# Kernel optimization log

Measured on AMD Instinct MI355X. Metric: run time of the kernel, lower is better.

The kernel has to match this reference:

```python
import jax, jax.numpy as jnp
import numpy as np
import math

B, N, F_IN, F_OUT = 8, 2048, 128, 128


def _uniform(key, shape, stdv):
    return jax.random.uniform(key, shape, dtype=jnp.float32, minval=-stdv, maxval=stdv)


def setup_inputs() -> dict:
    key = jax.random.key(0)
    k_x, k_a, k_w, k_att, k_bw, k_ba = jax.random.split(key, 6)
    X = jax.random.normal(k_x, (B, N, F_IN), dtype=jnp.float32)
    # dense 0/1 adjacency, as consumed by torch.bmm(A, ...)
    A = jax.random.randint(k_a, (B, N, N), 0, 2).astype(jnp.float32)
    stdv_W = 1.0 / math.sqrt(F_OUT)        # W.size(1) == n_fea_out
    stdv_a = 1.0 / math.sqrt(2 * F_OUT)    # a.size(1) == 2*n_fea_out
    W = _uniform(k_w, (F_IN, F_OUT), stdv_W)
    a = _uniform(k_att, (1, 2 * F_OUT), stdv_a)
    bias_W = _uniform(k_bw, (F_OUT,), stdv_W)
    bias_a = _uniform(k_ba, (N,), stdv_a)
    return {"X": X, "A": A, "W": W, "a": a, "bias_a": bias_a, "bias_W": bias_W}


def reference(X, A, W, a, bias_a, bias_W):
    # XW: [B, N, F_out]
    XW = jnp.einsum('bnf,fo->bno', X, W)
    f = W.shape[1]
    # Original materializes Z[b,i,j] = concat(XW[b,j], XW[b,i]) then dots with a.
    # This is separable: Z1[b,i,j] = a[:f]@XW[b,j] + a[f:]@XW[b,i] + bias_a[j]
    a_j = a[0, :f]   # multiplies XW[b, j]
    a_i = a[0, f:]   # multiplies XW[b, i]
    s_j = jnp.einsum('bnf,f->bn', XW, a_j)  # [B, N]
    s_i = jnp.einsum('bnf,f->bn', XW, a_i)  # [B, N]
    Z1 = s_i[:, :, None] + s_j[:, None, :] + bias_a[None, None, :]  # [B, N, N]
    den = jnp.exp(Z1)
    num = jnp.einsum('bik,bkj->bij', A, den)  # torch.bmm(A, denominator)
    # where numerator == 0 the torch code leaves att uninitialized; use 0 deterministically
    nz = num != 0
    att = jnp.where(nz, den / jnp.where(nz, num, 1.0), 0.0)
    buf = jnp.einsum('bij,bjf->bif', att, XW)
    H = jnp.einsum('bij,bjf->bif', A, buf) + bias_W
    return H
```

## Files before the change

kernel.cpp:

```cpp
#include <hip/hip_runtime.h>

#define BB 8
#define NN 2048
#define FF 128


__global__ __launch_bounds__(256) void k1_p_xsum(const float* __restrict__ X,
                                                 const float* __restrict__ W,
                                                 const float* __restrict__ av,
                                                 float* __restrict__ p,
                                                 float* __restrict__ xpart) {
    __shared__ float wls[FF];
    __shared__ float xls[FF];
    const int t = threadIdx.x;
    if (t < FF) {
        const float4* W4 = (const float4*)(W + t * FF);
        const float4* a4 = (const float4*)(av + FF);
        float s = 0.f;
#pragma unroll
        for (int f = 0; f < FF / 4; ++f) {
            const float4 w4 = W4[f], aa = a4[f];
            s += w4.x * aa.x + w4.y * aa.y + w4.z * aa.z + w4.w * aa.w;
        }
        wls[t] = s;
        xls[t] = 0.f;
    }
    __syncthreads();

    const int gr0 = blockIdx.x * 32;
    const int lane = t & 63, wave = t >> 6;
    const int half = lane >> 5, l32 = lane & 31;
    const float4 wv = ((const float4*)wls)[l32];
    float4 cs = make_float4(0.f, 0.f, 0.f, 0.f);
    const float4* X4 = (const float4*)(X + (size_t)gr0 * FF);

#pragma unroll
    for (int it = 0; it < 4; ++it) {
        const int rloc = wave * 8 + it * 2 + half;
        const float4 xv = X4[(size_t)rloc * 32 + l32];
        cs.x += xv.x; cs.y += xv.y; cs.z += xv.z; cs.w += xv.w;
        float s = xv.x * wv.x + xv.y * wv.y + xv.z * wv.z + xv.w * wv.w;
#pragma unroll
        for (int off = 16; off; off >>= 1) s += __shfl_xor(s, off, 64);
        if (l32 == 0) p[gr0 + rloc] = expf(s);
    }

    atomicAdd(&xls[l32 * 4 + 0], cs.x);
    atomicAdd(&xls[l32 * 4 + 1], cs.y);
    atomicAdd(&xls[l32 * 4 + 2], cs.z);
    atomicAdd(&xls[l32 * 4 + 3], cs.w);
    __syncthreads();
    if (t < FF) xpart[blockIdx.x * FF + t] = xls[t];
}

__global__ __launch_bounds__(256) void k3_r(const float* __restrict__ A,
                                            const float* __restrict__ W,
                                            const float* __restrict__ xpart,
                                            const float* __restrict__ p,
                                            float* __restrict__ r,
                                            float* __restrict__ S,
                                            unsigned* __restrict__ pk) {
    __shared__ float p_lds[NN];
    const int t = threadIdx.x;

    if (blockIdx.x == 0) {
#pragma unroll
        for (int k = 0; k < 4; ++k) {
            const int o = t + 256 * k;
            const int b = o >> 7, f = o & 127;
            float s = 0.f;
            for (int j = 0; j < 64; ++j) s += xpart[(b * 64 + j) * FF + f];
            p_lds[o] = s;
        }
        __syncthreads();
#pragma unroll
        for (int k = 0; k < 4; ++k) {
            const int o = t + 256 * k;
            const int b = o >> 7, f = o & 127;
            float s = 0.f;
#pragma unroll 8
            for (int c = 0; c < FF; ++c) s += p_lds[b * FF + c] * W[c * FF + f];
            S[o] = s;
        }
        return;
    }

    const int row0 = (blockIdx.x - 1) * 8;
    const int b = row0 >> 11;
    const float4* p4 = (const float4*)(p + (size_t)b * NN);
    float4* pl4 = (float4*)p_lds;
    pl4[t]       = p4[t];
    pl4[t + 256] = p4[t + 256];
    __syncthreads();

    const int lane = t & 63, wave = t >> 6;
    const int rowA = row0 + wave * 2;
    const int rowB = rowA + 1;
    const float4* Aa = (const float4*)(A + (size_t)rowA * NN);
    const float4* Ab = (const float4*)(A + (size_t)rowB * NN);

    const float4 va0 = Aa[0 * 64 + lane], va1 = Aa[1 * 64 + lane];
    const float4 va2 = Aa[2 * 64 + lane], va3 = Aa[3 * 64 + lane];
    const float4 va4 = Aa[4 * 64 + lane], va5 = Aa[5 * 64 + lane];
    const float4 va6 = Aa[6 * 64 + lane], va7 = Aa[7 * 64 + lane];
    const float4 vb0 = Ab[0 * 64 + lane], vb1 = Ab[1 * 64 + lane];
    const float4 vb2 = Ab[2 * 64 + lane], vb3 = Ab[3 * 64 + lane];
    const float4 vb4 = Ab[4 * 64 + lane], vb5 = Ab[5 * 64 + lane];
    const float4 vb6 = Ab[6 * 64 + lane], vb7 = Ab[7 * 64 + lane];
    __builtin_amdgcn_sched_barrier(0);

    float accA = 0.f, accB = 0.f;
    unsigned mA = 0u, mB = 0u;
#define STEP(K, VA, VB) {                                                     \
        const float4 pv = pl4[K * 64 + lane];                                 \
        accA += VA.x * pv.x + VA.y * pv.y + VA.z * pv.z + VA.w * pv.w;        \
        accB += VB.x * pv.x + VB.y * pv.y + VB.z * pv.z + VB.w * pv.w;        \
        const unsigned na = (VA.x != 0.f ? 1u : 0u) | (VA.y != 0.f ? 2u : 0u) \
                          | (VA.z != 0.f ? 4u : 0u) | (VA.w != 0.f ? 8u : 0u);\
        const unsigned nb = (VB.x != 0.f ? 1u : 0u) | (VB.y != 0.f ? 2u : 0u) \
                          | (VB.z != 0.f ? 4u : 0u) | (VB.w != 0.f ? 8u : 0u);\
        mA |= na << (K * 4); mB |= nb << (K * 4); }
    STEP(0, va0, vb0) STEP(1, va1, vb1) STEP(2, va2, vb2) STEP(3, va3, vb3)
    STEP(4, va4, vb4) STEP(5, va5, vb5) STEP(6, va6, vb6) STEP(7, va7, vb7)
#undef STEP

    pk[(size_t)rowA * 64 + lane] = mA;
    pk[(size_t)rowB * 64 + lane] = mB;

#pragma unroll
    for (int off = 32; off; off >>= 1) {
        accA += __shfl_xor(accA, off, 64);
        accB += __shfl_xor(accB, off, 64);
    }
    if (lane == 0) {
        const int lr = rowA & (NN - 1);
        r[rowA] = (accA != 0.f) ? (p_lds[lr] / accA) : 0.f;
        r[rowB] = (accB != 0.f) ? (p_lds[lr + 1] / accB) : 0.f;
    }
}

__global__ __launch_bounds__(256) void k4_H(const unsigned* __restrict__ pk,
                                            const float* __restrict__ rr,
                                            const float* __restrict__ S,
                                            const float* __restrict__ bias_W,
                                            float* __restrict__ Hout) {
    __shared__ float r_lds[NN];
    __shared__ float sls[FF], bwls[FF];
    const int t = threadIdx.x;
    const int row0 = blockIdx.x * 8;
    const int b = row0 >> 11;

    const float4* r4 = (const float4*)(rr + (size_t)b * NN);
    float4* rl4 = (float4*)r_lds;
    rl4[t]       = r4[t];
    rl4[t + 256] = r4[t + 256];
    if (t < FF) { sls[t] = S[b * FF + t]; bwls[t] = bias_W[t]; }
    __syncthreads();

    const int lane = t & 63, wave = t >> 6;
    const int rowA = row0 + wave * 2;
    const int rowB = rowA + 1;
    const unsigned wA = pk[(size_t)rowA * 64 + lane];
    const unsigned wB = pk[(size_t)rowB * 64 + lane];

    float accA = 0.f, accB = 0.f;
#pragma unroll
    for (int it = 0; it < 8; ++it) {
        const float4 rv = rl4[it * 64 + lane];
        const unsigned na = (wA >> (it * 4)) & 15u;
        const unsigned nb = (wB >> (it * 4)) & 15u;
        accA += (na & 1u) ? rv.x : 0.f;  accB += (nb & 1u) ? rv.x : 0.f;
        accA += (na & 2u) ? rv.y : 0.f;  accB += (nb & 2u) ? rv.y : 0.f;
        accA += (na & 4u) ? rv.z : 0.f;  accB += (nb & 4u) ? rv.z : 0.f;
        accA += (na & 8u) ? rv.w : 0.f;  accB += (nb & 8u) ? rv.w : 0.f;
    }
#pragma unroll
    for (int off = 32; off; off >>= 1) {
        accA += __shfl_xor(accA, off, 64);
        accB += __shfl_xor(accB, off, 64);
    }

    const float2 sv = ((const float2*)sls)[lane];
    const float2 bv = ((const float2*)bwls)[lane];
    float2* H2 = (float2*)Hout;
    H2[(size_t)rowA * 64 + lane] = make_float2(accA * sv.x + bv.x, accA * sv.y + bv.y);
    H2[(size_t)rowB * 64 + lane] = make_float2(accB * sv.x + bv.x, accB * sv.y + bv.y);
}

extern "C" void kernel_launch(void* const* d_in, const int* in_sizes, int n_in,
                              void* d_out, int out_size, void* d_ws, size_t ws_size,
                              hipStream_t stream) {
    const float* X      = (const float*)d_in[0];
    const float* A      = (const float*)d_in[1];
    const float* W      = (const float*)d_in[2];
    const float* a      = (const float*)d_in[3];
    const float* bias_W = (const float*)d_in[5];
    float* out = (float*)d_out;

    float* ws    = (float*)d_ws;
    float* xpart = ws;
    float* S     = ws + 65536;
    float* p     = ws + 66560;
    float* r     = ws + 82944;
    unsigned* pk = (unsigned*)(ws + 99328);

    k1_p_xsum<<<(BB * NN) / 32, 256, 0, stream>>>(X, W, a, p, xpart);
    k3_r<<<(BB * NN) / 8 + 1, 256, 0, stream>>>(A, W, xpart, p, r, S, pk);
    k4_H<<<(BB * NN) / 8, 256, 0, stream>>>(pk, r, S, bias_W, out);
}
```

Measured before the change: 227.5 us.

## Move adjacency bit-packing into first kernel; second kernel reads packed masks

The dense adjacency read and its conversion to bitmasks now happen in the first kernel, together with the p/xsum computation, which now uses 16 rows per block. The row-normalization kernel reads the 32x smaller packed masks instead of the full fp32 adjacency, so it no longer depends on the big read. The xpart reduction is resized to 128 partials per batch and workspace offsets are shifted. Total traffic over A is unchanged, so any gain depends on better overlap or occupancy from spreading the heavy read differently across kernels.

```diff
diff --git a/kernel.cpp b/kernel.cpp
--- a/kernel.cpp
+++ b/kernel.cpp
@@ -5,11 +5,13 @@
 #define FF 128
 
 
-__global__ __launch_bounds__(256) void k1_p_xsum(const float* __restrict__ X,
+__global__ __launch_bounds__(256) void kA_pack_p(const float* __restrict__ X,
+                                                 const float* __restrict__ A,
                                                  const float* __restrict__ W,
                                                  const float* __restrict__ av,
                                                  float* __restrict__ p,
-                                                 float* __restrict__ xpart) {
+                                                 float* __restrict__ xpart,
+                                                 unsigned* __restrict__ pk) {
     __shared__ float wls[FF];
     __shared__ float xls[FF];
     const int t = threadIdx.x;
@@ -27,39 +29,68 @@
     }
     __syncthreads();
 
-    const int gr0 = blockIdx.x * 32;
+    const int blk = blockIdx.x;
+    const int row0 = blk * 16;
     const int lane = t & 63, wave = t >> 6;
     const int half = lane >> 5, l32 = lane & 31;
-    const float4 wv = ((const float4*)wls)[l32];
-    float4 cs = make_float4(0.f, 0.f, 0.f, 0.f);
-    const float4* X4 = (const float4*)(X + (size_t)gr0 * FF);
-
-#pragma unroll
-    for (int it = 0; it < 4; ++it) {
-        const int rloc = wave * 8 + it * 2 + half;
-        const float4 xv = X4[(size_t)rloc * 32 + l32];
-        cs.x += xv.x; cs.y += xv.y; cs.z += xv.z; cs.w += xv.w;
-        float s = xv.x * wv.x + xv.y * wv.y + xv.z * wv.z + xv.w * wv.w;
-#pragma unroll
-        for (int off = 16; off; off >>= 1) s += __shfl_xor(s, off, 64);
-        if (l32 == 0) p[gr0 + rloc] = expf(s);
-    }
-
-    atomicAdd(&xls[l32 * 4 + 0], cs.x);
-    atomicAdd(&xls[l32 * 4 + 1], cs.y);
-    atomicAdd(&xls[l32 * 4 + 2], cs.z);
-    atomicAdd(&xls[l32 * 4 + 3], cs.w);
-    __syncthreads();
-    if (t < FF) xpart[blockIdx.x * FF + t] = xls[t];
-}
-
-__global__ __launch_bounds__(256) void k3_r(const float* __restrict__ A,
-                                            const float* __restrict__ W,
+
+    {
+        const float4 wv = ((const float4*)wls)[l32];
+        float4 cs = make_float4(0.f, 0.f, 0.f, 0.f);
+        const float4* X4 = (const float4*)(X + (size_t)row0 * FF);
+#pragma unroll
+        for (int k = 0; k < 2; ++k) {
+            const int rloc = wave * 4 + k * 2 + half;
+            const float4 xv = X4[rloc * 32 + l32];
+            cs.x += xv.x; cs.y += xv.y; cs.z += xv.z; cs.w += xv.w;
+            float s = xv.x * wv.x + xv.y * wv.y + xv.z * wv.z + xv.w * wv.w;
+#pragma unroll
+            for (int off = 16; off; off >>= 1) s += __shfl_xor(s, off, 64);
+            if (l32 == 0) p[row0 + rloc] = expf(s);
+        }
+        atomicAdd(&xls[l32 * 4 + 0], cs.x);
+        atomicAdd(&xls[l32 * 4 + 1], cs.y);
+        atomicAdd(&xls[l32 * 4 + 2], cs.z);
+        atomicAdd(&xls[l32 * 4 + 3], cs.w);
+    }
+    __syncthreads();
+    if (t < FF) xpart[blk * FF + t] = xls[t];
+
+    const int rbase = row0 + wave * 4;
+#pragma unroll 1
+    for (int g = 0; g < 2; ++g) {
+        const int rowA = rbase + g * 2;
+        const int rowB = rowA + 1;
+        const float4* Aa = (const float4*)(A + (size_t)rowA * NN);
+        const float4* Ab = (const float4*)(A + (size_t)rowB * NN);
+        const float4 va0 = Aa[0 * 64 + lane], va1 = Aa[1 * 64 + lane];
+        const float4 va2 = Aa[2 * 64 + lane], va3 = Aa[3 * 64 + lane];
+        const float4 va4 = Aa[4 * 64 + lane], va5 = Aa[5 * 64 + lane];
+        const float4 va6 = Aa[6 * 64 + lane], va7 = Aa[7 * 64 + lane];
+        const float4 vb0 = Ab[0 * 64 + lane], vb1 = Ab[1 * 64 + lane];
+        const float4 vb2 = Ab[2 * 64 + lane], vb3 = Ab[3 * 64 + lane];
+        const float4 vb4 = Ab[4 * 64 + lane], vb5 = Ab[5 * 64 + lane];
+        const float4 vb6 = Ab[6 * 64 + lane], vb7 = Ab[7 * 64 + lane];
+        __builtin_amdgcn_sched_barrier(0);
+        unsigned mA = 0u, mB = 0u;
+#define NIB(v) ((v.x != 0.f ? 1u : 0u) | (v.y != 0.f ? 2u : 0u) | \
+                (v.z != 0.f ? 4u : 0u) | (v.w != 0.f ? 8u : 0u))
+        mA |= NIB(va0) << 0;  mA |= NIB(va1) << 4;  mA |= NIB(va2) << 8;  mA |= NIB(va3) << 12;
+        mA |= NIB(va4) << 16; mA |= NIB(va5) << 20; mA |= NIB(va6) << 24; mA |= NIB(va7) << 28;
+        mB |= NIB(vb0) << 0;  mB |= NIB(vb1) << 4;  mB |= NIB(vb2) << 8;  mB |= NIB(vb3) << 12;
+        mB |= NIB(vb4) << 16; mB |= NIB(vb5) << 20; mB |= NIB(vb6) << 24; mB |= NIB(vb7) << 28;
+#undef NIB
+        pk[(size_t)rowA * 64 + lane] = mA;
+        pk[(size_t)rowB * 64 + lane] = mB;
+    }
+}
+
+__global__ __launch_bounds__(256) void kB_r(const float* __restrict__ W,
                                             const float* __restrict__ xpart,
                                             const float* __restrict__ p,
+                                            const unsigned* __restrict__ pk,
                                             float* __restrict__ r,
-                                            float* __restrict__ S,
-                                            unsigned* __restrict__ pk) {
+                                            float* __restrict__ S) {
     __shared__ float p_lds[NN];
     const int t = threadIdx.x;
 
@@ -69,7 +100,7 @@
             const int o = t + 256 * k;
             const int b = o >> 7, f = o & 127;
             float s = 0.f;
-            for (int j = 0; j < 64; ++j) s += xpart[(b * 64 + j) * FF + f];
+            for (int j = 0; j < 128; ++j) s += xpart[(b * 128 + j) * FF + f];
             p_lds[o] = s;
         }
         __syncthreads();
@@ -96,37 +127,20 @@
     const int lane = t & 63, wave = t >> 6;
     const int rowA = row0 + wave * 2;
     const int rowB = rowA + 1;
-    const float4* Aa = (const float4*)(A + (size_t)rowA * NN);
-    const float4* Ab = (const float4*)(A + (size_t)rowB * NN);
-
-    const float4 va0 = Aa[0 * 64 + lane], va1 = Aa[1 * 64 + lane];
-    const float4 va2 = Aa[2 * 64 + lane], va3 = Aa[3 * 64 + lane];
-    const float4 va4 = Aa[4 * 64 + lane], va5 = Aa[5 * 64 + lane];
-    const float4 va6 = Aa[6 * 64 + lane], va7 = Aa[7 * 64 + lane];
-    const float4 vb0 = Ab[0 * 64 + lane], vb1 = Ab[1 * 64 + lane];
-    const float4 vb2 = Ab[2 * 64 + lane], vb3 = Ab[3 * 64 + lane];
-    const float4 vb4 = Ab[4 * 64 + lane], vb5 = Ab[5 * 64 + lane];
-    const float4 vb6 = Ab[6 * 64 + lane], vb7 = Ab[7 * 64 + lane];
-    __builtin_amdgcn_sched_barrier(0);
+    const unsigned wA = pk[(size_t)rowA * 64 + lane];
+    const unsigned wB = pk[(size_t)rowB * 64 + lane];
 
     float accA = 0.f, accB = 0.f;
-    unsigned mA = 0u, mB = 0u;
-#define STEP(K, VA, VB) {                                                     \
-        const float4 pv = pl4[K * 64 + lane];                                 \
-        accA += VA.x * pv.x + VA.y * pv.y + VA.z * pv.z + VA.w * pv.w;        \
-        accB += VB.x * pv.x + VB.y * pv.y + VB.z * pv.z + VB.w * pv.w;        \
-        const unsigned na = (VA.x != 0.f ? 1u : 0u) | (VA.y != 0.f ? 2u : 0u) \
-                          | (VA.z != 0.f ? 4u : 0u) | (VA.w != 0.f ? 8u : 0u);\
-        const unsigned nb = (VB.x != 0.f ? 1u : 0u) | (VB.y != 0.f ? 2u : 0u) \
-                          | (VB.z != 0.f ? 4u : 0u) | (VB.w != 0.f ? 8u : 0u);\
-        mA |= na << (K * 4); mB |= nb << (K * 4); }
-    STEP(0, va0, vb0) STEP(1, va1, vb1) STEP(2, va2, vb2) STEP(3, va3, vb3)
-    STEP(4, va4, vb4) STEP(5, va5, vb5) STEP(6, va6, vb6) STEP(7, va7, vb7)
-#undef STEP
-
-    pk[(size_t)rowA * 64 + lane] = mA;
-    pk[(size_t)rowB * 64 + lane] = mB;
-
+#pragma unroll
+    for (int it = 0; it < 8; ++it) {
+        const float4 pv = pl4[it * 64 + lane];
+        const unsigned na = (wA >> (it * 4)) & 15u;
+        const unsigned nb = (wB >> (it * 4)) & 15u;
+        accA += (na & 1u) ? pv.x : 0.f;  accB += (nb & 1u) ? pv.x : 0.f;
+        accA += (na & 2u) ? pv.y : 0.f;  accB += (nb & 2u) ? pv.y : 0.f;
+        accA += (na & 4u) ? pv.z : 0.f;  accB += (nb & 4u) ? pv.z : 0.f;
+        accA += (na & 8u) ? pv.w : 0.f;  accB += (nb & 8u) ? pv.w : 0.f;
+    }
 #pragma unroll
     for (int off = 32; off; off >>= 1) {
         accA += __shfl_xor(accA, off, 64);
@@ -139,7 +153,7 @@
     }
 }
 
-__global__ __launch_bounds__(256) void k4_H(const unsigned* __restrict__ pk,
+__global__ __launch_bounds__(256) void kC_H(const unsigned* __restrict__ pk,
                                             const float* __restrict__ rr,
                                             const float* __restrict__ S,
                                             const float* __restrict__ bias_W,
@@ -199,12 +213,12 @@
 
     float* ws    = (float*)d_ws;
     float* xpart = ws;
-    float* S     = ws + 65536;
-    float* p     = ws + 66560;
-    float* r     = ws + 82944;
-    unsigned* pk = (unsigned*)(ws + 99328);
-
-    k1_p_xsum<<<(BB * NN) / 32, 256, 0, stream>>>(X, W, a, p, xpart);
-    k3_r<<<(BB * NN) / 8 + 1, 256, 0, stream>>>(A, W, xpart, p, r, S, pk);
-    k4_H<<<(BB * NN) / 8, 256, 0, stream>>>(pk, r, S, bias_W, out);
-}
+    float* S     = ws + 131072;
+    float* p     = ws + 132096;
+    float* r     = ws + 148480;
+    unsigned* pk = (unsigned*)(ws + 164864);
+
+    kA_pack_p<<<(BB * NN) / 16, 256, 0, stream>>>(X, A, W, a, p, xpart, pk);
+    kB_r<<<(BB * NN) / 8 + 1, 256, 0, stream>>>(W, xpart, p, pk, r, S);
+    kC_H<<<(BB * NN) / 8, 256, 0, stream>>>(pk, r, S, bias_W, out);
+}
```

New measurement: 241.0 us. 5.9% more time.
